# Performance work log

Hardware: AMD Instinct MI355X
Metric: run time of the kernel (lower is better)

Reference implementation:

```python
import jax, jax.numpy as jnp
import numpy as np

Q, B, D = 512, 4, 1024      # qlen, batch, d_model
L, H, DH, DI = 4, 16, 64, 4096  # layers, heads, d_head, d_inner
M = 512                      # mem_len


def setup_inputs() -> dict:
    key = jax.random.key(0)
    ks = jax.random.split(key, 10)
    w = lambda i, shape: jax.random.normal(ks[i], shape, jnp.float32) * 0.02
    return dict(
        x=jax.random.normal(ks[0], (Q, B, D), jnp.float32),
        mems=jax.random.normal(ks[1], (L, M, B, D), jnp.float32),
        u=w(2, (H, DH)),
        v=w(3, (H, DH)),
        W_qkv=w(4, (L, D, 3 * H * DH)),
        W_o=w(5, (L, H * DH, D)),
        W_r=w(6, (L, D, H * DH)),
        ln1_g=jnp.ones((L, D), jnp.float32),
        ln1_b=jnp.zeros((L, D), jnp.float32),
        W1=w(7, (L, D, DI)),
        b1=jnp.zeros((L, DI), jnp.float32),
        W2=w(8, (L, DI, D)),
        b2=jnp.zeros((L, D), jnp.float32),
        ln2_g=jnp.ones((L, D), jnp.float32),
        ln2_b=jnp.zeros((L, D), jnp.float32),
    )


def _layer_norm(x, g, b):
    mu = x.mean(-1, keepdims=True)
    var = ((x - mu) ** 2).mean(-1, keepdims=True)
    return (x - mu) * jax.lax.rsqrt(var + 1e-5) * g + b


def _rel_shift(x):
    # x: [q, k, b, n] -> Transformer-XL relative shift
    q, k, b, n = x.shape
    x = jnp.pad(x, ((0, 0), (1, 0), (0, 0), (0, 0)))
    return x.reshape(k + 1, q, b, n)[1:].reshape(q, k, b, n)


def _pos_emb(klen, d):
    pos = jnp.arange(klen - 1, -1, -1.0, dtype=jnp.float32)
    inv_freq = 1.0 / (10000.0 ** (jnp.arange(0, d, 2, dtype=jnp.float32) / d))
    ang = pos[:, None] * inv_freq[None, :]
    return jnp.concatenate([jnp.sin(ang), jnp.cos(ang)], axis=-1)  # [klen, d]


def reference(x, mems, u, v, W_qkv, W_o, W_r, ln1_g, ln1_b, W1, b1, W2, b2, ln2_g, ln2_b):
    q_len, bsz, d = x.shape
    mlen = mems.shape[1]
    klen = mlen + q_len
    r = _pos_emb(klen, d)                       # [klen, d]
    scale = 1.0 / np.sqrt(DH)
    # causal mask with memory: query i may attend key j iff j - i <= mlen
    mask = (jnp.arange(klen)[None, :] - jnp.arange(q_len)[:, None]) > mlen  # [q, k]
    h = x
    for i in range(L):
        cat = jnp.concatenate([mems[i], h], axis=0)       # [klen, b, d]
        heads = cat @ W_qkv[i]                            # [klen, b, 3*H*DH]
        qh, kh, vh = jnp.split(heads, 3, axis=-1)
        qh = qh[-q_len:].reshape(q_len, bsz, H, DH)
        kh = kh.reshape(klen, bsz, H, DH)
        vh = vh.reshape(klen, bsz, H, DH)
        rk = (r @ W_r[i]).reshape(klen, H, DH)            # [klen, H, DH]
        AC = jnp.einsum('ibnd,jbnd->ijbn', qh + u, kh)
        BD = _rel_shift(jnp.einsum('ibnd,jnd->ijbn', qh + v, rk))
        score = (AC + BD) * scale                         # [q, k, b, n]
        score = jnp.where(mask[:, :, None, None], -1e30, score)
        attn = jax.nn.softmax(score, axis=1)
        av = jnp.einsum('ijbn,jbnd->ibnd', attn, vh).reshape(q_len, bsz, H * DH)
        h = _layer_norm(h + av @ W_o[i], ln1_g[i], ln1_b[i])
        ff = jax.nn.relu(h @ W1[i] + b1[i]) @ W2[i] + b2[i]
        h = _layer_norm(h + ff, ln2_g[i], ln2_b[i])
    return h  # [qlen, bsz, d_model]
```

## Files before the change

### kernel.cpp

```cpp
#include <hip/hip_runtime.h>
#include <hip/hip_bf16.h>
#include <cstdint>
#include <cmath>

#define QL      512
#define BS      4
#define DMODEL  1024
#define NL      4
#define NH      16
#define DHEAD   64
#define DINNER  4096
#define MLEN    512
#define KLEN_   1024
#define HD_     1024
#define THD     3072
#define ROWS_H   2048

typedef __attribute__((ext_vector_type(8))) __bf16 bf16x8;
typedef __attribute__((ext_vector_type(4))) __bf16 bf16x4;
typedef __attribute__((ext_vector_type(4))) float  f32x4;

enum EpiMode { EPI_F32 = 0, EPI_BF16 = 1, EPI_RELU_BF16 = 2 };

#define SCL 0.18033688011112042f

__device__ __forceinline__ void glds16(const void* g, void* l) {
  __builtin_amdgcn_global_load_lds(
      (const __attribute__((address_space(1))) unsigned int*)g,
      (__attribute__((address_space(3))) unsigned int*)l, 16, 0, 0);
}

template<int BM, int BN, int WMT, int WNT, int EPI>
__global__ __launch_bounds__(256) void gemm_bt(
    const __bf16* __restrict__ A, const __bf16* __restrict__ Bt,
    void* __restrict__ Cv, const float* __restrict__ bias,
    int K, int lda, int ldb, int ldc,
    long sA, long Bn, long Cn)
{
  constexpr int WCOLS = BN / (WNT * 16);
  constexpr int WROWS = BM / (WMT * 16);
  static_assert(WCOLS * WROWS == 4, "must be 4 waves");
  __shared__ __align__(16) char smem[(BM + BN) * 64];
  char* sAm = smem;
  char* sBm = smem + BM * 64;

  const int bz = blockIdx.z;
  A  += (size_t)bz * sA;
  Bt += (size_t)bz * Bn;
  const size_t coff = (size_t)bz * Cn;

  const int tid  = threadIdx.x;
  const int wave = tid >> 6, lane = tid & 63;
  const int quad = lane >> 4, mrow = lane & 15;
  const int wr = wave / WCOLS, wc = wave % WCOLS;
  const int bm0 = blockIdx.x * BM, bn0 = blockIdx.y * BN;

  const int srow = lane >> 2;
  const int skq  = (lane & 3) ^ (srow & 3);
  const __bf16* gA = A  + (size_t)(bm0 + wave * (BM / 64) * 16 + srow) * lda + skq * 8;
  const __bf16* gB = Bt + (size_t)(bn0 + wave * (BN / 64) * 16 + srow) * ldb + skq * 8;
  char* lA = sAm + wave * (BM / 64) * 1024;
  char* lB = sBm + wave * (BN / 64) * 1024;

  const int aswz = (quad ^ (mrow & 3)) << 4;

  const f32x4 zero = {0.f, 0.f, 0.f, 0.f};
  f32x4 acc[WMT][WNT];
#pragma unroll
  for (int a = 0; a < WMT; ++a)
#pragma unroll
    for (int b = 0; b < WNT; ++b) acc[a][b] = zero;

  for (int k0 = 0; k0 < K; k0 += 32) {
#pragma unroll
    for (int p = 0; p < BM / 64; ++p)
      glds16(gA + (size_t)p * 16 * lda + k0, lA + p * 1024);
#pragma unroll
    for (int p = 0; p < BN / 64; ++p)
      glds16(gB + (size_t)p * 16 * ldb + k0, lB + p * 1024);
    __syncthreads();
    bf16x8 afr[WMT], bfr[WNT];
#pragma unroll
    for (int mt = 0; mt < WMT; ++mt)
      afr[mt] = *(const bf16x8*)(sAm + (wr * (WMT * 16) + mt * 16 + mrow) * 64 + aswz);
#pragma unroll
    for (int nt = 0; nt < WNT; ++nt)
      bfr[nt] = *(const bf16x8*)(sBm + (wc * (WNT * 16) + nt * 16 + mrow) * 64 + aswz);
#pragma unroll
    for (int mt = 0; mt < WMT; ++mt)
#pragma unroll
      for (int nt = 0; nt < WNT; ++nt)
        acc[mt][nt] = __builtin_amdgcn_mfma_f32_16x16x32_bf16(afr[mt], bfr[nt], acc[mt][nt], 0, 0, 0);
    __syncthreads();
  }

#pragma unroll
  for (int mt = 0; mt < WMT; ++mt) {
#pragma unroll
    for (int nt = 0; nt < WNT; ++nt) {
#pragma unroll
      for (int rr = 0; rr < 4; ++rr) {
        int gm = bm0 + wr * (WMT * 16) + mt * 16 + quad * 4 + rr;
        int gn = bn0 + wc * (WNT * 16) + nt * 16 + mrow;
        float val = acc[mt][nt][rr];
        if constexpr (EPI == EPI_F32) {
          ((float*)Cv)[coff + (size_t)gm * ldc + gn] = val;
        } else if constexpr (EPI == EPI_BF16) {
          ((__bf16*)Cv)[coff + (size_t)gm * ldc + gn] = (__bf16)val;
        } else {
          val += bias[gn];
          ((__bf16*)Cv)[coff + (size_t)gm * ldc + gn] = (__bf16)fmaxf(val, 0.f);
        }
      }
    }
  }
}

__global__ __launch_bounds__(256) void flash_attn(
    const __bf16* __restrict__ qu,
    const __bf16* __restrict__ qv,
    const __bf16* __restrict__ heads,
    const __bf16* __restrict__ rk,
    const __bf16* __restrict__ vt,
    __bf16* __restrict__ avp,
    float* __restrict__ mlpart)
{
  __shared__ __align__(16) char kh_t[64 * 144];
  __shared__ __align__(16) char rv_t[64 * 144];
  __shared__ float raw[64 * 132];

  const int wgid = blockIdx.x;
  const int xcd  = wgid & 7;
  const int slotw = wgid >> 3;
  const int bn   = ((slotw >> 4) << 3) + xcd;
  const int inner = slotw & 15;
  const int t    = 7 - (inner & 7);
  const int z    = inner >> 3;
  const int i0   = t * 64;
  const int b    = bn >> 4, n = bn & 15;
  const int nt   = t + 9;
  const int h    = (nt + 1) >> 1;
  const int ks   = z ? h : 0;
  const int ke   = z ? nt : h;

  const int tid = threadIdx.x;
  const int wave = tid >> 6, lane = tid & 63;
  const int quad = lane >> 4, mrow = lane & 15;
  const f32x4 zero = {0.f, 0.f, 0.f, 0.f};

  const __bf16* qub = qu + (size_t)bn * QL * DHEAD;
  const __bf16* qvb = qv + (size_t)bn * QL * DHEAD;
  const int qrow = i0 + wave * 16 + mrow;
  bf16x8 quf0 = *(const bf16x8*)(qub + (size_t)qrow * 64 + quad * 8);
  bf16x8 quf1 = *(const bf16x8*)(qub + (size_t)qrow * 64 + 32 + quad * 8);
  bf16x8 qvf0 = *(const bf16x8*)(qvb + (size_t)qrow * 64 + quad * 8);
  bf16x8 qvf1 = *(const bf16x8*)(qvb + (size_t)qrow * 64 + 32 + quad * 8);

  f32x4 o[4];
#pragma unroll
  for (int dt = 0; dt < 4; ++dt) o[dt] = zero;
  float m_r[4], l_r[4];
#pragma unroll
  for (int rr = 0; rr < 4; ++rr) { m_r[rr] = -3.0e38f; l_r[rr] = 0.f; }

  const int sr = tid >> 3;
  const int sc = (tid & 7) * 8;

  const __bf16* vtb = vt + (size_t)bn * (DHEAD * KLEN_);

  const int c0 = 448 - i0;
  const int cpre = c0 + 64 * ks;
#pragma unroll
  for (int p = 0; p < 2; ++p) {
    int r = p * 32 + sr;
    bf16x8 vv = *(const bf16x8*)(rk + (size_t)(cpre + r) * HD_ + n * 64 + sc);
    *(bf16x8*)(rv_t + r * 144 + sc * 2) = vv;
  }
  __syncthreads();
  {
    int slotc = ((cpre >> 6) & 1) * 64;
    __builtin_amdgcn_s_setprio(1);
#pragma unroll
    for (int ct = 0; ct < 4; ++ct) {
      bf16x8 b0 = *(const bf16x8*)(rv_t + (ct * 16 + mrow) * 144 + quad * 16);
      bf16x8 b1 = *(const bf16x8*)(rv_t + (ct * 16 + mrow) * 144 + 64 + quad * 16);
      f32x4 r = __builtin_amdgcn_mfma_f32_16x16x32_bf16(qvf0, b0, zero, 0, 0, 0);
      r = __builtin_amdgcn_mfma_f32_16x16x32_bf16(qvf1, b1, r, 0, 0, 0);
#pragma unroll
      for (int rr = 0; rr < 4; ++rr)
        raw[(wave * 16 + quad * 4 + rr) * 132 + slotc + ct * 16 + mrow] = r[rr];
    }
    __builtin_amdgcn_s_setprio(0);
  }
  bf16x8 kreg0, kreg1, rreg0, rreg1, vreg0, vreg1;
  {
    int j0 = ks * 64;
    kreg0 = *(const bf16x8*)(heads + (size_t)((j0 + sr) * BS + b) * THD + HD_ + n * 64 + sc);
    kreg1 = *(const bf16x8*)(heads + (size_t)((j0 + 32 + sr) * BS + b) * THD + HD_ + n * 64 + sc);
    int c1 = c0 + 64 * (ks + 1);
    if (c1 < KLEN_) {
      rreg0 = *(const bf16x8*)(rk + (size_t)(c1 + sr) * HD_ + n * 64 + sc);
      rreg1 = *(const bf16x8*)(rk + (size_t)(c1 + 32 + sr) * HD_ + n * 64 + sc);
    }
  }
  __syncthreads();

  const int i_base = i0 + wave * 16 + quad * 4;
  for (int k = ks; k < ke; ++k) {
    const int j0 = k * 64;
    const int cw = c0 + 64 * (k + 1);
    vreg0 = *(const bf16x8*)(vtb + (size_t)sr * KLEN_ + j0 + sc);
    vreg1 = *(const bf16x8*)(vtb + (size_t)(32 + sr) * KLEN_ + j0 + sc);
    *(bf16x8*)(kh_t + sr * 144 + sc * 2) = kreg0;
    *(bf16x8*)(kh_t + (32 + sr) * 144 + sc * 2) = kreg1;
    if (cw < KLEN_) {
      *(bf16x8*)(rv_t + sr * 144 + sc * 2) = rreg0;
      *(bf16x8*)(rv_t + (32 + sr) * 144 + sc * 2) = rreg1;
    }
    __syncthreads();
    __builtin_amdgcn_s_setprio(1);
    if (cw < KLEN_) {
      int slotc = ((cw >> 6) & 1) * 64;
#pragma unroll
      for (int ct = 0; ct < 4; ++ct) {
        bf16x8 b0 = *(const bf16x8*)(rv_t + (ct * 16 + mrow) * 144 + quad * 16);
        bf16x8 b1 = *(const bf16x8*)(rv_t + (ct * 16 + mrow) * 144 + 64 + quad * 16);
        f32x4 r = __builtin_amdgcn_mfma_f32_16x16x32_bf16(qvf0, b0, zero, 0, 0, 0);
        r = __builtin_amdgcn_mfma_f32_16x16x32_bf16(qvf1, b1, r, 0, 0, 0);
#pragma unroll
        for (int rr = 0; rr < 4; ++rr)
          raw[(wave * 16 + quad * 4 + rr) * 132 + slotc + ct * 16 + mrow] = r[rr];
      }
    }
    f32x4 s[4];
#pragma unroll
    for (int ct = 0; ct < 4; ++ct) {
      bf16x8 b0 = *(const bf16x8*)(kh_t + (ct * 16 + mrow) * 144 + quad * 16);
      bf16x8 b1 = *(const bf16x8*)(kh_t + (ct * 16 + mrow) * 144 + 64 + quad * 16);
      s[ct] = __builtin_amdgcn_mfma_f32_16x16x32_bf16(quf0, b0, zero, 0, 0, 0);
      s[ct] = __builtin_amdgcn_mfma_f32_16x16x32_bf16(quf1, b1, s[ct], 0, 0, 0);
    }
    __builtin_amdgcn_s_setprio(0);
    __syncthreads();
    if (k + 1 < ke) {
      int j1 = (k + 1) * 64;
      kreg0 = *(const bf16x8*)(heads + (size_t)((j1 + sr) * BS + b) * THD + HD_ + n * 64 + sc);
      kreg1 = *(const bf16x8*)(heads + (size_t)((j1 + 32 + sr) * BS + b) * THD + HD_ + n * 64 + sc);
      int cn2 = c0 + 64 * (k + 2);
      if (cn2 < KLEN_) {
        rreg0 = *(const bf16x8*)(rk + (size_t)(cn2 + sr) * HD_ + n * 64 + sc);
        rreg1 = *(const bf16x8*)(rk + (size_t)(cn2 + 32 + sr) * HD_ + n * 64 + sc);
      }
    }
    *(bf16x8*)(rv_t + sr * 144 + sc * 2) = vreg0;
    *(bf16x8*)(rv_t + (32 + sr) * 144 + sc * 2) = vreg1;
#pragma unroll
    for (int ct = 0; ct < 4; ++ct) {
#pragma unroll
      for (int rr = 0; rr < 4; ++rr) {
        int i = i_base + rr;
        int j = j0 + ct * 16 + mrow;
        float val;
        if (j - i <= MLEN) {
          int c = j - i + (QL - 1);
          int col = ((c >> 6) & 1) * 64 + (c & 63);
          val = (s[ct][rr] + raw[(wave * 16 + quad * 4 + rr) * 132 + col]) * SCL;
        } else val = -3.0e38f;
        s[ct][rr] = val;
      }
    }
    float alpha[4];
#pragma unroll
    for (int rr = 0; rr < 4; ++rr) {
      float mx = fmaxf(fmaxf(s[0][rr], s[1][rr]), fmaxf(s[2][rr], s[3][rr]));
#pragma unroll
      for (int off = 1; off < 16; off <<= 1) mx = fmaxf(mx, __shfl_xor(mx, off));
      float m_new = fmaxf(m_r[rr], mx);
      alpha[rr] = exp2f(m_r[rr] - m_new);
      m_r[rr] = m_new;
      float rs = 0.f;
#pragma unroll
      for (int ct = 0; ct < 4; ++ct) {
        float pv = exp2f(s[ct][rr] - m_new);
        s[ct][rr] = pv;
        rs += pv;
      }
#pragma unroll
      for (int off = 1; off < 16; off <<= 1) rs += __shfl_xor(rs, off);
      l_r[rr] = l_r[rr] * alpha[rr] + rs;
    }
#pragma unroll
    for (int dt = 0; dt < 4; ++dt)
#pragma unroll
      for (int rr = 0; rr < 4; ++rr) o[dt][rr] *= alpha[rr];
#pragma unroll
    for (int ct = 0; ct < 4; ++ct)
#pragma unroll
      for (int rr = 0; rr < 4; ++rr)
        ((__bf16*)kh_t)[(wave * 16 + quad * 4 + rr) * 72 + ct * 16 + mrow] = (__bf16)s[ct][rr];
    __syncthreads();
    {
      bf16x8 pf0 = *(const bf16x8*)(kh_t + (wave * 16 + mrow) * 144 + quad * 16);
      bf16x8 pf1 = *(const bf16x8*)(kh_t + (wave * 16 + mrow) * 144 + 64 + quad * 16);
      __builtin_amdgcn_s_setprio(1);
#pragma unroll
      for (int dt = 0; dt < 4; ++dt) {
        bf16x8 vf0 = *(const bf16x8*)(rv_t + (dt * 16 + mrow) * 144 + quad * 16);
        bf16x8 vf1 = *(const bf16x8*)(rv_t + (dt * 16 + mrow) * 144 + 64 + quad * 16);
        o[dt] = __builtin_amdgcn_mfma_f32_16x16x32_bf16(pf0, vf0, o[dt], 0, 0, 0);
        o[dt] = __builtin_amdgcn_mfma_f32_16x16x32_bf16(pf1, vf1, o[dt], 0, 0, 0);
      }
      __builtin_amdgcn_s_setprio(0);
    }
    __syncthreads();
  }

  const size_t prow = ((size_t)z * 64 + bn) * 512;
#pragma unroll
  for (int rr = 0; rr < 4; ++rr) {
    int i = i_base + rr;
    float inv = 1.0f / l_r[rr];
#pragma unroll
    for (int dt = 0; dt < 4; ++dt)
      avp[(prow + i) * 64 + dt * 16 + mrow] = (__bf16)(o[dt][rr] * inv);
  }
  if (mrow == 0) {
#pragma unroll
    for (int rr = 0; rr < 4; ++rr) {
      int i = i_base + rr;
      mlpart[(prow + i) * 2]     = m_r[rr];
      mlpart[(prow + i) * 2 + 1] = l_r[rr];
    }
  }
}

__global__ __launch_bounds__(256) void attn_combine(
    const __bf16* __restrict__ avp, const float* __restrict__ mlpart,
    __bf16* __restrict__ av)
{
  int idx = blockIdx.x * 256 + threadIdx.x;
  int dq = idx & 15;
  int i  = (idx >> 4) & 511;
  int bn = idx >> 13;
  int b = bn >> 4, n = bn & 15;
  size_t r0 = (size_t)bn * 512 + i;
  size_t r1 = r0 + (size_t)64 * 512;
  float m1 = mlpart[r0 * 2], l1 = mlpart[r0 * 2 + 1];
  float m2 = mlpart[r1 * 2], l2 = mlpart[r1 * 2 + 1];
  float m  = fmaxf(m1, m2);
  float w1 = l1 * exp2f(m1 - m), w2 = l2 * exp2f(m2 - m);
  float inv = 1.0f / (w1 + w2);
  w1 *= inv; w2 *= inv;
  bf16x4 o1 = *(const bf16x4*)(avp + r0 * 64 + dq * 4);
  bf16x4 o2 = *(const bf16x4*)(avp + r1 * 64 + dq * 4);
  bf16x4 ov;
#pragma unroll
  for (int j = 0; j < 4; ++j)
    ov[j] = (__bf16)((float)o1[j] * w1 + (float)o2[j] * w2);
  *(bf16x4*)(av + ((size_t)i * BS + b) * HD_ + n * 64 + dq * 4) = ov;
}


__global__ __launch_bounds__(256) void transpose_f32_bf16(
    const float* __restrict__ in, unsigned short* __restrict__ out, int R, int C)
{
  __shared__ float tile[64][66];
  int c0 = blockIdx.x * 64, r0 = blockIdx.y * 64;
  int tx = threadIdx.x, ty = threadIdx.y;
#pragma unroll
  for (int s = 0; s < 8; ++s) {
    int r = ty + s * 8;
    const float* p = in + (size_t)(r0 + r) * C + c0 + 2 * tx;
    tile[r][2 * tx]     = p[0];
    tile[r][2 * tx + 1] = p[1];
  }
  __syncthreads();
#pragma unroll
  for (int s = 0; s < 8; ++s) {
    int c = ty + s * 8;
    __bf16 lo = (__bf16)tile[2 * tx][c];
    __bf16 hi = (__bf16)tile[2 * tx + 1][c];
    unsigned int w = (unsigned int)*(unsigned short*)&lo |
                     ((unsigned int)*(unsigned short*)&hi << 16);
    *(unsigned int*)(out + (size_t)(c0 + c) * R + r0 + 2 * tx) = w;
  }
}

__global__ __launch_bounds__(256) void cast_f32_bf16(const float* __restrict__ in,
                                                     __bf16* __restrict__ out, int n)
{
  int i = blockIdx.x * 256 + threadIdx.x;
  if (i < n) out[i] = (__bf16)in[i];
}

__global__ __launch_bounds__(256) void posemb_kernel(__bf16* __restrict__ r)
{
  int idx = blockIdx.x * 256 + threadIdx.x;
  int p = idx >> 10, c = idx & 1023;
  int t = c & 511;
  float invf = __expf(-((float)t / 512.0f) * 9.210340371976184f);
  float ang = (float)(KLEN_ - 1 - p) * invf;
  float val = (c < 512) ? sinf(ang) : cosf(ang);
  r[idx] = (__bf16)val;
}

__global__ __launch_bounds__(256) void init_h(const float* __restrict__ x,
                                              float* __restrict__ hm,
                                              __bf16* __restrict__ hbf, int n)
{
  int i = blockIdx.x * 256 + threadIdx.x;
  if (i < n) { float t = x[i]; hm[i] = t; hbf[i] = (__bf16)t; }
}

__global__ __launch_bounds__(256) void build_quqv(const __bf16* __restrict__ heads,
                                                  const float* __restrict__ u,
                                                  const float* __restrict__ v,
                                                  __bf16* __restrict__ qu,
                                                  __bf16* __restrict__ qv)
{
  int idx = blockIdx.x * 256 + threadIdx.x;
  int d = idx & 63;
  int i = (idx >> 6) & (QL - 1);
  int bn = idx >> 15;
  int b = bn >> 4, n = bn & 15;
  float q = (float)heads[(size_t)((MLEN + i) * BS + b) * THD + n * 64 + d];
  int ud = n * 64 + d;
  qu[idx] = (__bf16)(q + u[ud]);
  qv[idx] = (__bf16)(q + v[ud]);
}

__global__ __launch_bounds__(256) void build_vt(const unsigned short* __restrict__ heads,
                                                unsigned short* __restrict__ vt)
{
  __shared__ unsigned short tile[64][65];
  int bn = blockIdx.y; int b = bn >> 4, n = bn & 15;
  int j0 = blockIdx.x * 64;
  int tx = threadIdx.x, ty = threadIdx.y;
#pragma unroll
  for (int s = 0; s < 16; ++s) {
    int j = ty + s * 4;
    tile[j][tx] = heads[(size_t)((j0 + j) * BS + b) * THD + 2048 + n * 64 + tx];
  }
  __syncthreads();
#pragma unroll
  for (int s = 0; s < 16; ++s) {
    int d = ty + s * 4;
    vt[(size_t)bn * DHEAD * KLEN_ + (size_t)d * KLEN_ + j0 + tx] = tile[tx][d];
  }
}

__global__ __launch_bounds__(256) void ln_kernel(float* __restrict__ hm,
                                                 const float* __restrict__ d0,
                                                 const float* __restrict__ d1,
                                                 const float* __restrict__ bias,
                                                 const float* __restrict__ g,
                                                 const float* __restrict__ b,
                                                 __bf16* __restrict__ hbf,
                                                 float* __restrict__ outf)
{
  int row = blockIdx.x;
  size_t base = (size_t)row * DMODEL;
  int tid = threadIdx.x;
  float x[4]; float sum = 0.f, sq = 0.f;
#pragma unroll
  for (int p = 0; p < 4; ++p) {
    int c = p * 256 + tid;
    float t = hm[base + c] + d0[base + c];
    if (d1) t += d1[base + c];
    if (bias) t += bias[c];
    x[p] = t; sum += t; sq += t * t;
  }
#pragma unroll
  for (int off = 32; off > 0; off >>= 1) { sum += __shfl_xor(sum, off); sq += __shfl_xor(sq, off); }
  __shared__ float rs[4], rq[4];
  int wave = tid >> 6, lane = tid & 63;
  if (lane == 0) { rs[wave] = sum; rq[wave] = sq; }
  __syncthreads();
  sum = rs[0] + rs[1] + rs[2] + rs[3];
  sq  = rq[0] + rq[1] + rq[2] + rq[3];
  float mu  = sum * (1.0f / DMODEL);
  float var = sq * (1.0f / DMODEL) - mu * mu;
  float rstd = rsqrtf(var + 1e-5f);
#pragma unroll
  for (int p = 0; p < 4; ++p) {
    int c = p * 256 + tid;
    float y = (x[p] - mu) * rstd * g[c] + b[c];
    hm[base + c] = y;
    hbf[base + c] = (__bf16)y;
    if (outf) outf[base + c] = y;
  }
}

extern "C" void kernel_launch(void* const* d_in, const int* in_sizes, int n_in,
                              void* d_out, int out_size, void* d_ws, size_t ws_size,
                              hipStream_t stream) {
  (void)in_sizes; (void)n_in; (void)out_size; (void)ws_size;
  const float* x    = (const float*)d_in[0];
  const float* mems = (const float*)d_in[1];
  const float* u    = (const float*)d_in[2];
  const float* v    = (const float*)d_in[3];
  const float* Wqkv = (const float*)d_in[4];
  const float* Wo   = (const float*)d_in[5];
  const float* Wr   = (const float*)d_in[6];
  const float* ln1g = (const float*)d_in[7];
  const float* ln1b = (const float*)d_in[8];
  const float* W1   = (const float*)d_in[9];
  const float* b1   = (const float*)d_in[10];
  const float* W2   = (const float*)d_in[11];
  const float* b2   = (const float*)d_in[12];
  const float* ln2g = (const float*)d_in[13];
  const float* ln2b = (const float*)d_in[14];

  size_t off = 0;
  char* ws = (char*)d_ws;
  auto alloc = [&](size_t bytes) { size_t o = off; off += (bytes + 255) & ~(size_t)255; return o; };
  __bf16* wT    = (__bf16*)(ws + alloc((size_t)DINNER * DMODEL * 2));
  char*   R1    = (char*)(ws + alloc((size_t)(2 * ROWS_H) * THD * 2));
  __bf16* heads = (__bf16*)R1;
  float*  proj  = (float*)R1;
  __bf16* ff1   = (__bf16*)(R1 + (size_t)ROWS_H * DMODEL * 4);
  __bf16* catb  = (__bf16*)(ws + alloc((size_t)(2 * ROWS_H) * DMODEL * 2));
  __bf16* memsb = catb;
  __bf16* hbf   = catb + (size_t)ROWS_H * DMODEL;
  __bf16* av    = catb;
  float*  mlprt = (float*)hbf;
  __bf16* avp   = wT;
  __bf16* r_bf  = (__bf16*)(ws + alloc((size_t)KLEN_ * DMODEL * 2));
  __bf16* rk4   = (__bf16*)(ws + alloc((size_t)NL * KLEN_ * HD_ * 2));
  __bf16* qu    = (__bf16*)(ws + alloc((size_t)2 * BS * NH * QL * DHEAD * 2));
  __bf16* qv    = qu + (size_t)BS * NH * QL * DHEAD;
  float*  ff2p  = (float*)qu;
  __bf16* vt    = (__bf16*)(ws + alloc((size_t)BS * NH * DHEAD * KLEN_ * 2));
  float*  hm    = (float*)(ws + alloc((size_t)ROWS_H * DMODEL * 4));

  posemb_kernel<<<(KLEN_ * DMODEL) / 256, 256, 0, stream>>>(r_bf);
  init_h<<<(ROWS_H * DMODEL) / 256, 256, 0, stream>>>(x, hm, hbf, ROWS_H * DMODEL);

  for (int i = 0; i < NL; ++i)
    transpose_f32_bf16<<<dim3(HD_ / 64, DMODEL / 64), dim3(32, 8), 0, stream>>>(
        Wr + (size_t)i * DMODEL * HD_, (unsigned short*)(wT + (size_t)i * HD_ * DMODEL),
        DMODEL, HD_);
  gemm_bt<128, 128, 4, 4, EPI_BF16><<<dim3(8, 8, NL), 256, 0, stream>>>(
      r_bf, wT, rk4, nullptr, DMODEL, DMODEL, DMODEL, HD_,
      0, (long)HD_ * DMODEL, (long)KLEN_ * HD_);

  for (int i = 0; i < NL; ++i) {
    cast_f32_bf16<<<(MLEN * BS * DMODEL) / 256, 256, 0, stream>>>(
        mems + (size_t)i * MLEN * BS * DMODEL, memsb, MLEN * BS * DMODEL);
    transpose_f32_bf16<<<dim3(THD / 64, DMODEL / 64), dim3(32, 8), 0, stream>>>(
        Wqkv + (size_t)i * DMODEL * THD, (unsigned short*)wT, DMODEL, THD);
    gemm_bt<128, 128, 4, 4, EPI_BF16><<<dim3(32, 24, 1), 256, 0, stream>>>(
        catb, wT, heads, nullptr, DMODEL, DMODEL, DMODEL, THD, 0, 0, 0);

    build_quqv<<<(BS * NH * QL * DHEAD) / 256, 256, 0, stream>>>(heads, u, v, qu, qv);
    build_vt<<<dim3(KLEN_ / 64, BS * NH), dim3(64, 4), 0, stream>>>(
        (const unsigned short*)heads, (unsigned short*)vt);

    flash_attn<<<dim3(1024), 256, 0, stream>>>(
        qu, qv, heads, rk4 + (size_t)i * KLEN_ * HD_, vt, avp, mlprt);
    attn_combine<<<(64 * 512 * 16) / 256, 256, 0, stream>>>(avp, mlprt, av);

    transpose_f32_bf16<<<dim3(DMODEL / 64, HD_ / 64), dim3(32, 8), 0, stream>>>(
        Wo + (size_t)i * HD_ * DMODEL, (unsigned short*)wT, HD_, DMODEL);
    gemm_bt<128, 64, 4, 2, EPI_F32><<<dim3(16, 16, 1), 256, 0, stream>>>(
        av, wT, proj, nullptr, HD_, HD_, HD_, DMODEL, 0, 0, 0);
    ln_kernel<<<ROWS_H, 256, 0, stream>>>(hm, proj, nullptr, nullptr,
                                          ln1g + i * DMODEL, ln1b + i * DMODEL, hbf, nullptr);

    transpose_f32_bf16<<<dim3(DINNER / 64, DMODEL / 64), dim3(32, 8), 0, stream>>>(
        W1 + (size_t)i * DMODEL * DINNER, (unsigned short*)wT, DMODEL, DINNER);
    gemm_bt<128, 128, 4, 4, EPI_RELU_BF16><<<dim3(16, 32, 1), 256, 0, stream>>>(
        hbf, wT, ff1, b1 + i * DINNER, DMODEL, DMODEL, DMODEL, DINNER, 0, 0, 0);

    transpose_f32_bf16<<<dim3(DMODEL / 64, DINNER / 64), dim3(32, 8), 0, stream>>>(
        W2 + (size_t)i * DINNER * DMODEL, (unsigned short*)wT, DINNER, DMODEL);
    gemm_bt<128, 64, 4, 2, EPI_F32><<<dim3(16, 16, 2), 256, 0, stream>>>(
        ff1, wT, proj, nullptr, DINNER / 2, DINNER, DINNER, DMODEL,
        (long)(DINNER / 2), (long)(DINNER / 2), (long)(ff2p - proj));
    ln_kernel<<<ROWS_H, 256, 0, stream>>>(hm, proj, ff2p, b2 + i * DMODEL,
                                          ln2g + i * DMODEL, ln2b + i * DMODEL, hbf,
                                          (i == NL - 1) ? (float*)d_out : nullptr);
  }
}
```

Baseline: 1.235 ms.

## Unroll GEMM K-loop to 64 per sync and store BD scores as bf16

The GEMM kernel now loads two 32-wide K slices into separate LDS buffers per iteration, so each pair of barriers covers 64 K elements instead of 32. This halves the number of barrier round trips at the cost of doubling LDS per block. Separately, the attention kernel keeps its relative-position score scratch in bf16 instead of fp32, which shrinks LDS use and may raise occupancy. The bf16 scratch loses precision on the BD term before it is added and scaled.

```diff
diff --git a/kernel.cpp b/kernel.cpp
--- a/kernel.cpp
+++ b/kernel.cpp
@@ -40,9 +40,11 @@
   constexpr int WCOLS = BN / (WNT * 16);
   constexpr int WROWS = BM / (WMT * 16);
   static_assert(WCOLS * WROWS == 4, "must be 4 waves");
-  __shared__ __align__(16) char smem[(BM + BN) * 64];
-  char* sAm = smem;
-  char* sBm = smem + BM * 64;
+  __shared__ __align__(16) char smem[(BM + BN) * 128];
+  char* sA0 = smem;
+  char* sA1 = smem + BM * 64;
+  char* sB0 = smem + BM * 128;
+  char* sB1 = smem + BM * 128 + BN * 64;
 
   const int bz = blockIdx.z;
   A  += (size_t)bz * sA;
@@ -59,8 +61,10 @@
   const int skq  = (lane & 3) ^ (srow & 3);
   const __bf16* gA = A  + (size_t)(bm0 + wave * (BM / 64) * 16 + srow) * lda + skq * 8;
   const __bf16* gB = Bt + (size_t)(bn0 + wave * (BN / 64) * 16 + srow) * ldb + skq * 8;
-  char* lA = sAm + wave * (BM / 64) * 1024;
-  char* lB = sBm + wave * (BN / 64) * 1024;
+  char* lA0 = sA0 + wave * (BM / 64) * 1024;
+  char* lA1 = sA1 + wave * (BM / 64) * 1024;
+  char* lB0 = sB0 + wave * (BN / 64) * 1024;
+  char* lB1 = sB1 + wave * (BN / 64) * 1024;
 
   const int aswz = (quad ^ (mrow & 3)) << 4;
 
@@ -71,21 +75,36 @@
 #pragma unroll
     for (int b = 0; b < WNT; ++b) acc[a][b] = zero;
 
-  for (int k0 = 0; k0 < K; k0 += 32) {
-#pragma unroll
-    for (int p = 0; p < BM / 64; ++p)
-      glds16(gA + (size_t)p * 16 * lda + k0, lA + p * 1024);
-#pragma unroll
-    for (int p = 0; p < BN / 64; ++p)
-      glds16(gB + (size_t)p * 16 * ldb + k0, lB + p * 1024);
+  for (int k0 = 0; k0 < K; k0 += 64) {
+#pragma unroll
+    for (int p = 0; p < BM / 64; ++p) {
+      glds16(gA + (size_t)p * 16 * lda + k0,      lA0 + p * 1024);
+      glds16(gA + (size_t)p * 16 * lda + k0 + 32, lA1 + p * 1024);
+    }
+#pragma unroll
+    for (int p = 0; p < BN / 64; ++p) {
+      glds16(gB + (size_t)p * 16 * ldb + k0,      lB0 + p * 1024);
+      glds16(gB + (size_t)p * 16 * ldb + k0 + 32, lB1 + p * 1024);
+    }
     __syncthreads();
     bf16x8 afr[WMT], bfr[WNT];
 #pragma unroll
     for (int mt = 0; mt < WMT; ++mt)
-      afr[mt] = *(const bf16x8*)(sAm + (wr * (WMT * 16) + mt * 16 + mrow) * 64 + aswz);
+      afr[mt] = *(const bf16x8*)(sA0 + (wr * (WMT * 16) + mt * 16 + mrow) * 64 + aswz);
 #pragma unroll
     for (int nt = 0; nt < WNT; ++nt)
-      bfr[nt] = *(const bf16x8*)(sBm + (wc * (WNT * 16) + nt * 16 + mrow) * 64 + aswz);
+      bfr[nt] = *(const bf16x8*)(sB0 + (wc * (WNT * 16) + nt * 16 + mrow) * 64 + aswz);
+#pragma unroll
+    for (int mt = 0; mt < WMT; ++mt)
+#pragma unroll
+      for (int nt = 0; nt < WNT; ++nt)
+        acc[mt][nt] = __builtin_amdgcn_mfma_f32_16x16x32_bf16(afr[mt], bfr[nt], acc[mt][nt], 0, 0, 0);
+#pragma unroll
+    for (int mt = 0; mt < WMT; ++mt)
+      afr[mt] = *(const bf16x8*)(sA1 + (wr * (WMT * 16) + mt * 16 + mrow) * 64 + aswz);
+#pragma unroll
+    for (int nt = 0; nt < WNT; ++nt)
+      bfr[nt] = *(const bf16x8*)(sB1 + (wc * (WNT * 16) + nt * 16 + mrow) * 64 + aswz);
 #pragma unroll
     for (int mt = 0; mt < WMT; ++mt)
 #pragma unroll
@@ -127,7 +146,7 @@
 {
   __shared__ __align__(16) char kh_t[64 * 144];
   __shared__ __align__(16) char rv_t[64 * 144];
-  __shared__ float raw[64 * 132];
+  __shared__ __align__(4) __bf16 rawb[64 * 134];
 
   const int wgid = blockIdx.x;
   const int xcd  = wgid & 7;
@@ -188,7 +207,7 @@
       r = __builtin_amdgcn_mfma_f32_16x16x32_bf16(qvf1, b1, r, 0, 0, 0);
 #pragma unroll
       for (int rr = 0; rr < 4; ++rr)
-        raw[(wave * 16 + quad * 4 + rr) * 132 + slotc + ct * 16 + mrow] = r[rr];
+        rawb[(wave * 16 + quad * 4 + rr) * 134 + slotc + ct * 16 + mrow] = (__bf16)r[rr];
     }
     __builtin_amdgcn_s_setprio(0);
   }
@@ -229,7 +248,7 @@
         r = __builtin_amdgcn_mfma_f32_16x16x32_bf16(qvf1, b1, r, 0, 0, 0);
 #pragma unroll
         for (int rr = 0; rr < 4; ++rr)
-          raw[(wave * 16 + quad * 4 + rr) * 132 + slotc + ct * 16 + mrow] = r[rr];
+          rawb[(wave * 16 + quad * 4 + rr) * 134 + slotc + ct * 16 + mrow] = (__bf16)r[rr];
       }
     }
     f32x4 s[4];
@@ -264,7 +283,7 @@
         if (j - i <= MLEN) {
           int c = j - i + (QL - 1);
           int col = ((c >> 6) & 1) * 64 + (c & 63);
-          val = (s[ct][rr] + raw[(wave * 16 + quad * 4 + rr) * 132 + col]) * SCL;
+          val = (s[ct][rr] + (float)rawb[(wave * 16 + quad * 4 + rr) * 134 + col]) * SCL;
         } else val = -3.0e38f;
         s[ct][rr] = val;
       }
```

Measured after the change: 1.132 ms. -8.3%, faster.
